# Kernel tuning notes

Measured on AMD Instinct MI355X. Metric: run time of the kernel, lower is better.

Reference implementation:

```python
import jax, jax.numpy as jnp
import numpy as np

H = 96  # LSTM units hardcoded in the module


def setup_inputs() -> dict:
    key = jax.random.key(0)
    ks = jax.random.split(key, 5)
    B, LAT, V = 32, 64, 10000
    z = jax.random.normal(ks[0], (B, LAT), dtype=jnp.float32)
    # Keras LSTM params: kernel [in,4H], recurrent_kernel [H,4H], bias [4H]; gate order i,f,c,o
    W = jax.random.normal(ks[1], (LAT, 4 * H), dtype=jnp.float32) * 0.05
    U = jax.random.normal(ks[2], (H, 4 * H), dtype=jnp.float32) * 0.05
    b = jnp.zeros((4 * H,), dtype=jnp.float32)
    Wd = jax.random.normal(ks[3], (H, V), dtype=jnp.float32) * 0.05
    bd = jnp.zeros((V,), dtype=jnp.float32)
    return {"z": z, "W": W, "U": U, "b": b, "Wd": Wd, "bd": bd, "seq_len": 512}


def reference(z, W, U, b, Wd, bd, seq_len):
    # RepeatVector: every timestep sees the same input z, so the input
    # projection z@W + b is computed once and reused across all T steps.
    zp = z @ W + b  # [B, 4H]
    B = z.shape[0]
    h0 = jnp.zeros((B, H), z.dtype)
    c0 = jnp.zeros((B, H), z.dtype)

    def step(carry, _):
        h, c = carry
        g = zp + h @ U  # [B, 4H]
        i = jax.nn.sigmoid(g[:, :H])
        f = jax.nn.sigmoid(g[:, H:2 * H])
        cbar = jnp.tanh(g[:, 2 * H:3 * H])
        o = jax.nn.sigmoid(g[:, 3 * H:])
        c = f * c + i * cbar
        h = o * jnp.tanh(c)
        return (h, c), h

    _, hs = jax.lax.scan(step, (h0, c0), None, length=seq_len)  # [T, B, H]
    hs = jnp.transpose(hs, (1, 0, 2))  # [B, T, H]
    logits = hs @ Wd + bd  # [B, T, V]
    return jax.nn.softmax(logits, axis=-1)
```

## Files before the change

### kernel.cpp

```cpp
#include <hip/hip_runtime.h>
#include <cmath>

#define B_SZ  32
#define LATD  64
#define HU    96
#define G4    384
#define T_LEN 512
#define VOC   10000
#define NROWS (B_SZ * T_LEN)
#define NC16  625
#define NSPLIT 5
#define C16S  125
#define RBLK  32
#define PPR   (NSPLIT * 2)
#define PACK_BLOCKS ((NC16 * 3 * 64) / 192)
#define LSTM_GRID   (B_SZ + PACK_BLOCKS)

typedef __attribute__((ext_vector_type(8))) short bf16x8;
typedef __attribute__((ext_vector_type(4))) float f32x4;

__device__ __forceinline__ unsigned short f2bf(float x) {
  unsigned u = __float_as_uint(x);
  u += 0x7fffu + ((u >> 16) & 1u);
  return (unsigned short)(u >> 16);
}
__device__ __forceinline__ float fsig(float x) {
  return __builtin_amdgcn_rcpf(1.f + __expf(-x));
}
__device__ __forceinline__ float ftanh(float x) {
  return 1.f - 2.f * __builtin_amdgcn_rcpf(1.f + __expf(2.f * x));
}

__global__ __launch_bounds__(192) void lstm_fused(
    const float* __restrict__ z, const float* __restrict__ W,
    const float* __restrict__ U, const float* __restrict__ bias,
    const float* __restrict__ Wd, unsigned short* __restrict__ hsb,
    uint4* __restrict__ Bp) {
  const int tid = threadIdx.x;

  if (blockIdx.x >= B_SZ) {
    const int gid = (blockIdx.x - B_SZ) * 192 + tid;
    const int l   = gid & 63;
    const int K16 = (gid >> 6) % 3;
    const int c16 = gid / 192;
    const int col = c16 * 16 + (l & 15);
    const int k0  = K16 * 32 + (l >> 4) * 8;
    unsigned wb[4];
#pragma unroll
    for (int jj = 0; jj < 4; ++jj) {
      float x0 = Wd[(size_t)(k0 + 2 * jj) * VOC + col];
      float x1 = Wd[(size_t)(k0 + 2 * jj + 1) * VOC + col];
      wb[jj] = (unsigned)f2bf(x0) | ((unsigned)f2bf(x1) << 16);
    }
    Bp[gid] = make_uint4(wb[0], wb[1], wb[2], wb[3]);
    return;
  }

  __shared__ __align__(16) unsigned short hbuf[2][HU];
  __shared__ float z_lds[LATD];
  const int bb = blockIdx.x;
  const int l  = tid & 63, wv = tid >> 6;
  const int c  = l & 15, kg = l >> 4, k0 = kg * 8;

  if (tid < LATD)   z_lds[tid] = z[bb * LATD + tid];
  if (tid < HU / 2) ((unsigned*)hbuf[0])[tid] = 0u;

  int cols[2][4];
#pragma unroll
  for (int u = 0; u < 2; ++u)
#pragma unroll
    for (int g = 0; g < 4; ++g) cols[u][g] = (6 * g + wv + 3 * u) * 16 + c;

  bf16x8 Ufr[2][4][3];
#pragma unroll
  for (int u = 0; u < 2; ++u)
#pragma unroll
    for (int g = 0; g < 4; ++g)
#pragma unroll
      for (int kt = 0; kt < 3; ++kt) {
        const int kb = kt * 32 + k0;
        unsigned wb[4];
#pragma unroll
        for (int jj = 0; jj < 4; ++jj) {
          float x0 = U[(size_t)(kb + 2 * jj) * G4 + cols[u][g]];
          float x1 = U[(size_t)(kb + 2 * jj + 1) * G4 + cols[u][g]];
          wb[jj] = (unsigned)f2bf(x0) | ((unsigned)f2bf(x1) << 16);
        }
        uint4 u4 = make_uint4(wb[0], wb[1], wb[2], wb[3]);
        Ufr[u][g][kt] = __builtin_bit_cast(bf16x8, u4);
      }

  float zp[2][4];
#pragma unroll
  for (int u = 0; u < 2; ++u)
#pragma unroll
    for (int g = 0; g < 4; ++g) zp[u][g] = bias[cols[u][g]];
  __syncthreads();
  for (int k = 0; k < LATD; ++k) {
    const float zk = z_lds[k];
    const float* wr = W + (size_t)k * G4;
#pragma unroll
    for (int u = 0; u < 2; ++u)
#pragma unroll
      for (int g = 0; g < 4; ++g) zp[u][g] = fmaf(zk, wr[cols[u][g]], zp[u][g]);
  }

  float cst[2] = {0.f, 0.f};
  unsigned short* hrow = hsb + (size_t)bb * T_LEN * HU;
  int p = 0;
  const f32x4 zero4 = {0.f, 0.f, 0.f, 0.f};
  const int u0 = c + 16 * wv, u1 = u0 + 48;

  for (int s = 0; s < T_LEN; ++s) {
    bf16x8 afr[3];
#pragma unroll
    for (int kt = 0; kt < 3; ++kt)
      afr[kt] = *(const bf16x8*)(&hbuf[p][kt * 32 + k0]);

    float gate[2][4];
#pragma unroll
    for (int u = 0; u < 2; ++u)
#pragma unroll
      for (int g = 0; g < 4; ++g) {
        f32x4 da = __builtin_amdgcn_mfma_f32_16x16x32_bf16(afr[0], Ufr[u][g][0], zero4, 0, 0, 0);
        da = __builtin_amdgcn_mfma_f32_16x16x32_bf16(afr[2], Ufr[u][g][2], da, 0, 0, 0);
        f32x4 db = __builtin_amdgcn_mfma_f32_16x16x32_bf16(afr[1], Ufr[u][g][1], zero4, 0, 0, 0);
        gate[u][g] = (da[0] + db[0]) + zp[u][g];
      }

    unsigned short hb[2];
#pragma unroll
    for (int u = 0; u < 2; ++u) {
      const float i_ = fsig(gate[u][0]);
      const float f_ = fsig(gate[u][1]);
      const float cb = ftanh(gate[u][2]);
      const float o_ = fsig(gate[u][3]);
      cst[u] = f_ * cst[u] + i_ * cb;
      hb[u] = f2bf(o_ * ftanh(cst[u]));
    }
    if (kg == 0)      hbuf[p ^ 1][u0] = hb[0];
    else if (kg == 3) hbuf[p ^ 1][u1] = hb[1];
    else if (kg == 1) hrow[(size_t)s * HU + u0] = hb[0];
    else              hrow[(size_t)s * HU + u1] = hb[1];
    __syncthreads();
    p ^= 1;
  }
}

template <int PASS>
__global__ __launch_bounds__(256) void dense_pass(
    const unsigned short* __restrict__ hsb, const bf16x8* __restrict__ Bp,
    const float* __restrict__ bd, const float* __restrict__ part,
    float* __restrict__ outp) {
  __shared__ __align__(16) unsigned short Al[RBLK * HU];
  const int tid = threadIdx.x;
  const int l = tid & 63, wv = tid >> 6;
  const int rt = wv & 1, cg = wv >> 1;
  const int l15 = l & 15, l4 = l >> 4;
  const int s = blockIdx.x / 512, rb = blockIdx.x % 512;
  const int R0 = rb * RBLK;

  {
    const uint4* src = (const uint4*)(hsb + (size_t)R0 * HU);
    uint4* dst = (uint4*)Al;
    for (int i = tid; i < RBLK * HU / 8; i += 256) dst[i] = src[i];
  }
  __syncthreads();

  bf16x8 afr[3];
#pragma unroll
  for (int kt = 0; kt < 3; ++kt)
    afr[kt] = *(const bf16x8*)(Al + (rt * 16 + l15) * HU + kt * 32 + l4 * 8);

  const int row = R0 + rt * 16 + l15;
  float iv = 0.f;
  if (PASS == 1) {
    float sum = 0.f;
#pragma unroll
    for (int i = 0; i < PPR; ++i) sum += part[(size_t)row * PPR + i];
    iv = 1.f / sum;
  }

  float srun = 0.f;
  for (int i = cg; i < C16S; i += 2) {
    const int c16 = s * C16S + i;
    const bf16x8* bp = Bp + (size_t)c16 * 192 + l;
    const bf16x8 b0 = bp[0], b1 = bp[64], b2 = bp[128];
    f32x4 acc = {0.f, 0.f, 0.f, 0.f};
    acc = __builtin_amdgcn_mfma_f32_16x16x32_bf16(b0, afr[0], acc, 0, 0, 0);
    acc = __builtin_amdgcn_mfma_f32_16x16x32_bf16(b1, afr[1], acc, 0, 0, 0);
    acc = __builtin_amdgcn_mfma_f32_16x16x32_bf16(b2, afr[2], acc, 0, 0, 0);
    const int colb = c16 * 16 + l4 * 4;
    const f32x4 bd4 = *(const f32x4*)(bd + colb);
    if (PASS == 0) {
#pragma unroll
      for (int q = 0; q < 4; ++q) srun += __expf(acc[q] + bd4[q]);
    } else {
      f32x4 o;
#pragma unroll
      for (int q = 0; q < 4; ++q) o[q] = __expf(acc[q] + bd4[q]) * iv;
      __builtin_nontemporal_store(o, (f32x4*)(outp + (size_t)row * VOC + colb));
    }
  }

  if (PASS == 0) {
    srun += __shfl_xor(srun, 16);
    srun += __shfl_xor(srun, 32);
    if (l4 == 0)
      ((float*)outp)[(size_t)row * PPR + s * 2 + cg] = srun;
  }
}

extern "C" void kernel_launch(void* const* d_in, const int* in_sizes, int n_in,
                              void* d_out, int out_size, void* d_ws, size_t ws_size,
                              hipStream_t stream) {
  const float* z  = (const float*)d_in[0];
  const float* W  = (const float*)d_in[1];
  const float* U  = (const float*)d_in[2];
  const float* b  = (const float*)d_in[3];
  const float* Wd = (const float*)d_in[4];
  const float* bd = (const float*)d_in[5];
  float* out = (float*)d_out;

  char* ws = (char*)d_ws;
  unsigned short* hsb = (unsigned short*)ws;
  uint4* Bp   = (uint4*)(ws + 3145728);
  float* part = (float*)(ws + 3145728 + 1920000);

  lstm_fused<<<LSTM_GRID, 192, 0, stream>>>(z, W, U, b, Wd, hsb, Bp);
  dense_pass<0><<<512 * NSPLIT, 256, 0, stream>>>(hsb, (const bf16x8*)Bp, bd,
                                                  nullptr, part);
  dense_pass<1><<<512 * NSPLIT, 256, 0, stream>>>(hsb, (const bf16x8*)Bp, bd,
                                                  part, out);
}
```

Measured before the change: 611.3 us.

## Double LSTM block width and buffer hidden states in an LDS ring

The recurrent kernel now runs 384 threads (6 waves) per batch row, so each wave handles one hidden-unit group instead of two. That halves the serial MFMA and activation work per wave on each step. Hidden states go into a 256-entry LDS ring and are written to global memory in bulk every 256 steps, instead of a scattered store every step. The cost is two larger block-wide flushes with an extra barrier, more LDS use, and 6-wave barriers on every step.

```diff
diff --git a/kernel.cpp b/kernel.cpp
--- a/kernel.cpp
+++ b/kernel.cpp
@@ -13,7 +13,8 @@
 #define C16S  125
 #define RBLK  32
 #define PPR   (NSPLIT * 2)
-#define PACK_BLOCKS ((NC16 * 3 * 64) / 192)
+#define HIST  256
+#define PACK_BLOCKS ((NC16 * 3 * 64 + 383) / 384)
 #define LSTM_GRID   (B_SZ + PACK_BLOCKS)
 
 typedef __attribute__((ext_vector_type(8))) short bf16x8;
@@ -31,7 +32,7 @@
   return 1.f - 2.f * __builtin_amdgcn_rcpf(1.f + __expf(2.f * x));
 }
 
-__global__ __launch_bounds__(192) void lstm_fused(
+__global__ __launch_bounds__(384) void lstm_fused(
     const float* __restrict__ z, const float* __restrict__ W,
     const float* __restrict__ U, const float* __restrict__ bias,
     const float* __restrict__ Wd, unsigned short* __restrict__ hsb,
@@ -39,111 +40,103 @@
   const int tid = threadIdx.x;
 
   if (blockIdx.x >= B_SZ) {
-    const int gid = (blockIdx.x - B_SZ) * 192 + tid;
-    const int l   = gid & 63;
-    const int K16 = (gid >> 6) % 3;
-    const int c16 = gid / 192;
-    const int col = c16 * 16 + (l & 15);
-    const int k0  = K16 * 32 + (l >> 4) * 8;
-    unsigned wb[4];
-#pragma unroll
-    for (int jj = 0; jj < 4; ++jj) {
-      float x0 = Wd[(size_t)(k0 + 2 * jj) * VOC + col];
-      float x1 = Wd[(size_t)(k0 + 2 * jj + 1) * VOC + col];
-      wb[jj] = (unsigned)f2bf(x0) | ((unsigned)f2bf(x1) << 16);
-    }
-    Bp[gid] = make_uint4(wb[0], wb[1], wb[2], wb[3]);
+    const int gid = (blockIdx.x - B_SZ) * 384 + tid;
+    if (gid < NC16 * 3 * 64) {
+      const int l   = gid & 63;
+      const int K16 = (gid >> 6) % 3;
+      const int c16 = gid / 192;
+      const int col = c16 * 16 + (l & 15);
+      const int k0  = K16 * 32 + (l >> 4) * 8;
+      unsigned wb[4];
+#pragma unroll
+      for (int jj = 0; jj < 4; ++jj) {
+        float x0 = Wd[(size_t)(k0 + 2 * jj) * VOC + col];
+        float x1 = Wd[(size_t)(k0 + 2 * jj + 1) * VOC + col];
+        wb[jj] = (unsigned)f2bf(x0) | ((unsigned)f2bf(x1) << 16);
+      }
+      Bp[gid] = make_uint4(wb[0], wb[1], wb[2], wb[3]);
+    }
     return;
   }
 
-  __shared__ __align__(16) unsigned short hbuf[2][HU];
+  __shared__ __align__(16) unsigned short hsring[HIST][HU];
   __shared__ float z_lds[LATD];
   const int bb = blockIdx.x;
   const int l  = tid & 63, wv = tid >> 6;
   const int c  = l & 15, kg = l >> 4, k0 = kg * 8;
 
-  if (tid < LATD)   z_lds[tid] = z[bb * LATD + tid];
-  if (tid < HU / 2) ((unsigned*)hbuf[0])[tid] = 0u;
-
-  int cols[2][4];
-#pragma unroll
-  for (int u = 0; u < 2; ++u)
-#pragma unroll
-    for (int g = 0; g < 4; ++g) cols[u][g] = (6 * g + wv + 3 * u) * 16 + c;
-
-  bf16x8 Ufr[2][4][3];
-#pragma unroll
-  for (int u = 0; u < 2; ++u)
-#pragma unroll
-    for (int g = 0; g < 4; ++g)
-#pragma unroll
-      for (int kt = 0; kt < 3; ++kt) {
-        const int kb = kt * 32 + k0;
-        unsigned wb[4];
-#pragma unroll
-        for (int jj = 0; jj < 4; ++jj) {
-          float x0 = U[(size_t)(kb + 2 * jj) * G4 + cols[u][g]];
-          float x1 = U[(size_t)(kb + 2 * jj + 1) * G4 + cols[u][g]];
-          wb[jj] = (unsigned)f2bf(x0) | ((unsigned)f2bf(x1) << 16);
-        }
-        uint4 u4 = make_uint4(wb[0], wb[1], wb[2], wb[3]);
-        Ufr[u][g][kt] = __builtin_bit_cast(bf16x8, u4);
+  if (tid < LATD) z_lds[tid] = z[bb * LATD + tid];
+  if (tid < 12)   ((uint4*)(hsring[HIST - 1]))[tid] = make_uint4(0u, 0u, 0u, 0u);
+
+  int cols[4];
+#pragma unroll
+  for (int g = 0; g < 4; ++g) cols[g] = (6 * g + wv) * 16 + c;
+
+  bf16x8 Ufr[4][3];
+#pragma unroll
+  for (int g = 0; g < 4; ++g) {
+#pragma unroll
+    for (int kt = 0; kt < 3; ++kt) {
+      const int kb = kt * 32 + k0;
+      unsigned wb[4];
+#pragma unroll
+      for (int jj = 0; jj < 4; ++jj) {
+        float x0 = U[(size_t)(kb + 2 * jj) * G4 + cols[g]];
+        float x1 = U[(size_t)(kb + 2 * jj + 1) * G4 + cols[g]];
+        wb[jj] = (unsigned)f2bf(x0) | ((unsigned)f2bf(x1) << 16);
       }
-
-  float zp[2][4];
-#pragma unroll
-  for (int u = 0; u < 2; ++u)
-#pragma unroll
-    for (int g = 0; g < 4; ++g) zp[u][g] = bias[cols[u][g]];
+      uint4 u4 = make_uint4(wb[0], wb[1], wb[2], wb[3]);
+      Ufr[g][kt] = __builtin_bit_cast(bf16x8, u4);
+    }
+  }
+
+  float zp[4];
+#pragma unroll
+  for (int g = 0; g < 4; ++g) zp[g] = bias[cols[g]];
   __syncthreads();
   for (int k = 0; k < LATD; ++k) {
     const float zk = z_lds[k];
     const float* wr = W + (size_t)k * G4;
 #pragma unroll
-    for (int u = 0; u < 2; ++u)
-#pragma unroll
-      for (int g = 0; g < 4; ++g) zp[u][g] = fmaf(zk, wr[cols[u][g]], zp[u][g]);
-  }
-
-  float cst[2] = {0.f, 0.f};
+    for (int g = 0; g < 4; ++g) zp[g] = fmaf(zk, wr[cols[g]], zp[g]);
+  }
+
+  float cst = 0.f;
   unsigned short* hrow = hsb + (size_t)bb * T_LEN * HU;
-  int p = 0;
   const f32x4 zero4 = {0.f, 0.f, 0.f, 0.f};
-  const int u0 = c + 16 * wv, u1 = u0 + 48;
+  const int u0 = c + 16 * wv;
 
   for (int s = 0; s < T_LEN; ++s) {
+    const int rs = (s + HIST - 1) & (HIST - 1);
     bf16x8 afr[3];
 #pragma unroll
     for (int kt = 0; kt < 3; ++kt)
-      afr[kt] = *(const bf16x8*)(&hbuf[p][kt * 32 + k0]);
-
-    float gate[2][4];
-#pragma unroll
-    for (int u = 0; u < 2; ++u)
-#pragma unroll
-      for (int g = 0; g < 4; ++g) {
-        f32x4 da = __builtin_amdgcn_mfma_f32_16x16x32_bf16(afr[0], Ufr[u][g][0], zero4, 0, 0, 0);
-        da = __builtin_amdgcn_mfma_f32_16x16x32_bf16(afr[2], Ufr[u][g][2], da, 0, 0, 0);
-        f32x4 db = __builtin_amdgcn_mfma_f32_16x16x32_bf16(afr[1], Ufr[u][g][1], zero4, 0, 0, 0);
-        gate[u][g] = (da[0] + db[0]) + zp[u][g];
-      }
-
-    unsigned short hb[2];
-#pragma unroll
-    for (int u = 0; u < 2; ++u) {
-      const float i_ = fsig(gate[u][0]);
-      const float f_ = fsig(gate[u][1]);
-      const float cb = ftanh(gate[u][2]);
-      const float o_ = fsig(gate[u][3]);
-      cst[u] = f_ * cst[u] + i_ * cb;
-      hb[u] = f2bf(o_ * ftanh(cst[u]));
-    }
-    if (kg == 0)      hbuf[p ^ 1][u0] = hb[0];
-    else if (kg == 3) hbuf[p ^ 1][u1] = hb[1];
-    else if (kg == 1) hrow[(size_t)s * HU + u0] = hb[0];
-    else              hrow[(size_t)s * HU + u1] = hb[1];
+      afr[kt] = *(const bf16x8*)(&hsring[rs][kt * 32 + k0]);
+
+    float g4[4];
+#pragma unroll
+    for (int g = 0; g < 4; ++g) {
+      f32x4 da = __builtin_amdgcn_mfma_f32_16x16x32_bf16(afr[0], Ufr[g][0], zero4, 0, 0, 0);
+      da = __builtin_amdgcn_mfma_f32_16x16x32_bf16(afr[2], Ufr[g][2], da, 0, 0, 0);
+      f32x4 db = __builtin_amdgcn_mfma_f32_16x16x32_bf16(afr[1], Ufr[g][1], zero4, 0, 0, 0);
+      g4[g] = (da[0] + db[0]) + zp[g];
+    }
+
+    const float i_ = fsig(g4[0]);
+    const float f_ = fsig(g4[1]);
+    const float cb = ftanh(g4[2]);
+    const float o_ = fsig(g4[3]);
+    cst = f_ * cst + i_ * cb;
+    const float h = o_ * ftanh(cst);
+    if (kg == 0) hsring[s & (HIST - 1)][u0] = f2bf(h);
     __syncthreads();
-    p ^= 1;
+
+    if ((s & (HIST - 1)) == (HIST - 1)) {
+      const uint4* srcp = (const uint4*)hsring;
+      uint4* dstp = (uint4*)(hrow + (size_t)(s - (HIST - 1)) * HU);
+      for (int i = tid; i < HIST * HU / 8; i += 384) dstp[i] = srcp[i];
+      __syncthreads();
+    }
   }
 }
 
@@ -227,7 +220,7 @@
   uint4* Bp   = (uint4*)(ws + 3145728);
   float* part = (float*)(ws + 3145728 + 1920000);
 
-  lstm_fused<<<LSTM_GRID, 192, 0, stream>>>(z, W, U, b, Wd, hsb, Bp);
+  lstm_fused<<<LSTM_GRID, 384, 0, stream>>>(z, W, U, b, Wd, hsb, Bp);
   dense_pass<0><<<512 * NSPLIT, 256, 0, stream>>>(hsb, (const bf16x8*)Bp, bd,
                                                   nullptr, part);
   dense_pass<1><<<512 * NSPLIT, 256, 0, stream>>>(hsb, (const bf16x8*)Bp, bd,
```

Result: faster. 516.1 us (-15.6%).
